# Optimization experiments

Hardware: AMD Instinct MI355X
Metric: run time of the kernel (lower is better)

Reference implementation:

```python
import jax, jax.numpy as jnp
import numpy as np

B, H, C, W = 16, 256, 128, 128  # input is (B, H, C_in, W); C_out = C_in = 128


def setup_inputs() -> dict:
    key = jax.random.key(0)
    ks = jax.random.split(key, 7)
    s = 0.02
    return {
        "x": jax.random.normal(ks[0], (B, H, C, W), dtype=jnp.float32),
        "Wq": jax.random.normal(ks[1], (C, C), dtype=jnp.float32) * s,
        "bq": jnp.zeros((C,), dtype=jnp.float32),
        "Wk": jax.random.normal(ks[2], (C, C), dtype=jnp.float32) * s,
        "bk": jnp.zeros((C,), dtype=jnp.float32),
        "Wv": jax.random.normal(ks[3], (C, C), dtype=jnp.float32) * s,
        "bv": jnp.zeros((C,), dtype=jnp.float32),
        "Wn": jax.random.normal(ks[4], (C, C), dtype=jnp.float32) * s,
        "bn": jnp.zeros((C,), dtype=jnp.float32),
        "Wo": jax.random.normal(ks[5], (C, C), dtype=jnp.float32) * s,
        "bo": jnp.zeros((C,), dtype=jnp.float32),
    }


def reference(x, Wq, bq, Wk, bk, Wv, bv, Wn, bn, Wo, bo):
    # x: (B, H, C, W) -> channels_first layout (B, C, H, W)
    xt = jnp.transpose(x, (0, 2, 1, 3))
    # 1x1 channels_first convs == channel-mixing GEMMs
    q = jnp.einsum('bchw,cd->bdhw', xt, Wq) + bq[None, :, None, None]
    k = jnp.einsum('bchw,cd->bdhw', xt, Wk) + bk[None, :, None, None]
    v = jnp.einsum('bchw,cd->bdhw', xt, Wv) + bv[None, :, None, None]
    # QK^T over H, laid out as (B, C, C', W); scale by sqrt(W) (= last dim of k)
    scale = jnp.sqrt(jnp.asarray(k.shape[-1], dtype=x.dtype))
    scores = jnp.einsum('bchw,bdhw->bcdw', q, k) / scale
    attn = jax.nn.softmax(scores, axis=-1)  # softmax over W axis (as in source)
    # DropConnect: identity at inference (training=None)
    # weight_norm: channels_last 1x1 conv mixing the second C axis
    wn = jnp.einsum('bcdw,de->bcew', attn, Wn) + bn[None, None, :, None]
    # attention-value matmul: out[b,c,h,w] = sum_d wn[b,c,d,w] * v[b,d,h,w]
    m = jnp.einsum('bcdw,bdhw->bchw', wn, v)
    # conv1: channels_first 1x1, C_in -> C_out
    out = jnp.einsum('bchw,co->bohw', m, Wo) + bo[None, :, None, None]
    # back to (B, H, C_out, W)
    return jnp.transpose(out, (0, 2, 1, 3))
```

## Files before the change

kernel.cpp:

```cpp
#include <hip/hip_runtime.h>
#include <cstddef>

#define BB 16
#define HH 256
#define CC 128
#define WW 128

typedef _Float16 f16;
typedef _Float16 f16x8 __attribute__((ext_vector_type(8)));
typedef _Float16 f16x4 __attribute__((ext_vector_type(4)));
typedef _Float16 f16x2 __attribute__((ext_vector_type(2)));
typedef float f32x4 __attribute__((ext_vector_type(4)));

#define LD1 136
#define LDX 264
#define REG 17920

__device__ __forceinline__ void zero_acc(f32x4 acc[4][4]) {
#pragma unroll
    for (int i = 0; i < 4; ++i)
#pragma unroll
        for (int j = 0; j < 4; ++j) acc[i][j] = (f32x4){0.f, 0.f, 0.f, 0.f};
}

__device__ __forceinline__ void gemm_ab(const f16* __restrict__ A, int lda,
                                        const f16* __restrict__ B, int ldb,
                                        int K, int m0, int n0, int l15, int quad,
                                        f32x4 acc[4][4]) {
    for (int kc = 0; kc < K; kc += 32) {
        f16x8 af[4], bf[4];
        const f16* ap = A + (size_t)(m0 + l15) * lda + kc + quad * 8;
        const f16* bp = B + (size_t)(n0 + l15) * ldb + kc + quad * 8;
#pragma unroll
        for (int t = 0; t < 4; ++t) {
            af[t] = *(const f16x8*)(ap + t * 16 * lda);
            bf[t] = *(const f16x8*)(bp + t * 16 * ldb);
        }
#pragma unroll
        for (int mt = 0; mt < 4; ++mt)
#pragma unroll
            for (int nt = 0; nt < 4; ++nt)
                acc[mt][nt] = __builtin_amdgcn_mfma_f32_16x16x32_f16(af[mt], bf[nt], acc[mt][nt], 0, 0, 0);
    }
}

__device__ __forceinline__ void gemm_a_btr(const f16* __restrict__ A, int lda,
                                           const f16* __restrict__ XS,
                                           int m0, int n0, int l15, int quad,
                                           f32x4 acc[4][4]) {
    const unsigned xb = (unsigned)(size_t)XS;
    for (int kc = 0; kc < 128; kc += 32) {
        f16x8 af[4];
        const f16* ap = A + (size_t)(m0 + l15) * lda + kc + quad * 8;
#pragma unroll
        for (int t = 0; t < 4; ++t) af[t] = *(const f16x8*)(ap + t * 16 * lda);
        int i0 = (kc >> 2) + 2 * quad;
        f16x4 blo[4], bhi[4];
#pragma unroll
        for (int nt = 0; nt < 4; ++nt) {
            unsigned idx0 = (unsigned)(i0 * 8 + (n0 >> 4) + nt);
            unsigned a0 = xb + (idx0 * 68u + (unsigned)l15 * 4u) * 2u;
            unsigned a1 = a0 + 8u * 68u * 2u;
            asm volatile("ds_read_b64_tr_b16 %0, %1" : "=v"(blo[nt]) : "v"(a0));
            asm volatile("ds_read_b64_tr_b16 %0, %1" : "=v"(bhi[nt]) : "v"(a1));
        }
        asm volatile("s_waitcnt lgkmcnt(0)" ::: "memory");
        __builtin_amdgcn_sched_barrier(0);
#pragma unroll
        for (int nt = 0; nt < 4; ++nt) {
            f16x8 bv = __builtin_shufflevector(blo[nt], bhi[nt], 0, 1, 2, 3, 4, 5, 6, 7);
#pragma unroll
            for (int mt = 0; mt < 4; ++mt)
                acc[mt][nt] = __builtin_amdgcn_mfma_f32_16x16x32_f16(af[mt], bv, acc[mt][nt], 0, 0, 0);
        }
    }
}

__device__ __forceinline__ void stage_ct(const f32x4 acc[4][4], f16* dst, int ld,
                                         int m0, int n0, int l15, int quad) {
#pragma unroll
    for (int mt = 0; mt < 4; ++mt)
#pragma unroll
        for (int nt = 0; nt < 4; ++nt) {
            f16x4 v;
#pragma unroll
            for (int r = 0; r < 4; ++r) v[r] = (f16)acc[mt][nt][r];
            int col = n0 + nt * 16 + l15;
            int row = m0 + mt * 16 + quad * 4;
            *(f16x4*)(dst + (size_t)col * ld + row) = v;
        }
}

__device__ __forceinline__ void stage_c_mirror(const f32x4 acc[4][4], f16* dst, int ld,
                                               int m0, int n0, int l15, int quad) {
#pragma unroll
    for (int mt = 0; mt < 4; ++mt)
#pragma unroll
        for (int r = 0; r < 4; ++r) {
            int row = m0 + mt * 16 + quad * 4 + r;
#pragma unroll
            for (int nt = 0; nt < 4; ++nt)
                dst[(size_t)row * ld + n0 + nt * 16 + l15] = (f16)acc[mt][nt][r];
        }
}

__device__ __forceinline__ void stage_ct_r1(const f32x4 acc[4][4], f16* dst, int ld,
                                            int m0, int n0, int l15, int quad,
                                            const float* __restrict__ gv,
                                            const float* __restrict__ wv) {
#pragma unroll
    for (int mt = 0; mt < 4; ++mt)
#pragma unroll
        for (int nt = 0; nt < 4; ++nt) {
            int col = n0 + nt * 16 + l15;
            int row0 = m0 + mt * 16 + quad * 4;
            float ws = wv[col];
            f16x4 v;
#pragma unroll
            for (int r = 0; r < 4; ++r) v[r] = (f16)(acc[mt][nt][r] + ws * gv[row0 + r]);
            *(f16x4*)(dst + (size_t)col * ld + row0) = v;
        }
}

__device__ __forceinline__ void stage_w(const f16* __restrict__ g, f16* dst, int tid) {
#pragma unroll
    for (int i = 0; i < 8; ++i) {
        int idx = tid + i * 256;
        int row = idx >> 4, cc = (idx & 15) * 8;
        *(f16x8*)(dst + row * LD1 + cc) = *(const f16x8*)(g + row * 128 + cc);
    }
}

__device__ __forceinline__ void load_w_reg(const f16* __restrict__ g, f16x8 wr[8], int tid) {
#pragma unroll
    for (int i = 0; i < 8; ++i) {
        int idx = tid + i * 256;
        wr[i] = *(const f16x8*)(g + (idx >> 4) * 128 + (idx & 15) * 8);
    }
}
__device__ __forceinline__ void stage_w_from_reg(const f16x8 wr[8], f16* dst, int tid) {
#pragma unroll
    for (int i = 0; i < 8; ++i) {
        int idx = tid + i * 256;
        *(f16x8*)(dst + (idx >> 4) * LD1 + (idx & 15) * 8) = wr[i];
    }
}
__device__ __forceinline__ void load_x_reg(const f16* __restrict__ g, f16x8 wr[8], int tid) {
#pragma unroll
    for (int i = 0; i < 8; ++i) {
        int idx = tid + i * 256;
        wr[i] = *(const f16x8*)(g + (idx >> 4) * 256 + (idx & 15) * 8);
    }
}
__device__ __forceinline__ void stage_x_from_reg(const f16x8 wr[8], f16* dst, int tid) {
#pragma unroll
    for (int i = 0; i < 8; ++i) {
        int idx = tid + i * 256;
        int c2 = idx >> 4, cc = (idx & 15) * 8;
        int off = ((c2 >> 2) * 8 + (cc >> 4)) * 68 + (c2 & 3) * 16 + (cc & 15);
        f16x4 lo, hi;
#pragma unroll
        for (int j = 0; j < 4; ++j) { lo[j] = wr[i][j]; hi[j] = wr[i][4 + j]; }
        *(f16x4*)(dst + off) = lo;
        *(f16x4*)(dst + off + 4) = hi;
    }
}

__global__ __launch_bounds__(256) void prep_w(const float* __restrict__ Wq, const float* __restrict__ Wk,
                                              const float* __restrict__ Wo, f16* __restrict__ out) {
    int id = blockIdx.x * 256 + threadIdx.x;
    int m = id >> 14;
    int r = (id >> 7) & 127, c = id & 127;
    if (m == 0)      out[id] = (f16)Wq[c * 128 + r];
    else if (m == 1) out[id] = (f16)Wk[c * 128 + r];
    else             out[4 * 16384 + (id & 16383)] = (f16)Wo[c * 128 + r];
}

__global__ __launch_bounds__(512) void prep_mv(const float* __restrict__ Wn, const float* __restrict__ Wv,
                                               const float* __restrict__ Wo, const float* __restrict__ bn,
                                               const float* __restrict__ bv,
                                               f16* __restrict__ Wpk, float* __restrict__ Vg) {
    __shared__ f16 As[128 * LD1];
    __shared__ f16 Bs[128 * LD1];
    const int tid = threadIdx.x;
    if (tid < 128) {
        float s = 0.f;
        for (int e = 0; e < 128; ++e) s = fmaf(Wn[tid * 128 + e], bv[e], s);
        Vg[tid] = s;
    } else if (tid < 256) {
        int c = tid - 128;
        float s = 0.f;
        for (int e = 0; e < 128; ++e) s = fmaf(bn[e], Wv[c * 128 + e], s);
        Vg[128 + c] = s;
    } else if (tid < 384) {
        int o = tid - 256;
        float s = 0.f;
        for (int c = 0; c < 128; ++c) s += Wo[c * 128 + o];
        Vg[256 + o] = s;
    } else if (tid == 384) {
        float s = 0.f;
        for (int e = 0; e < 128; ++e) s = fmaf(bn[e], bv[e], s);
        Vg[384] = s;
    }
    if (tid < 256) {
#pragma unroll
        for (int i = 0; i < 8; ++i) {
            int idx = tid + i * 256;
            int r = idx >> 4, c = (idx & 15) * 8;
            f16x8 va, vb;
            const float* pa = Wv + r * 128 + c;
            const float* pb = Wn + r * 128 + c;
#pragma unroll
            for (int j = 0; j < 8; ++j) { va[j] = (f16)pa[j]; vb[j] = (f16)pb[j]; }
            *(f16x8*)(As + r * LD1 + c) = va;
            *(f16x8*)(Bs + r * LD1 + c) = vb;
        }
    }
    __syncthreads();
    if (tid < 256) {
        const int lane = tid & 63, wid = tid >> 6;
        const int l15 = lane & 15, quad = lane >> 4;
        const int m0 = (wid >> 1) * 64, n0 = (wid & 1) * 64;
        f32x4 acc[4][4];
        zero_acc(acc);
        gemm_ab(As, LD1, Bs, LD1, 128, m0, n0, l15, quad, acc);
        f16* Mt = Wpk + 2 * 16384;
#pragma unroll
        for (int mt = 0; mt < 4; ++mt)
#pragma unroll
            for (int r = 0; r < 4; ++r) {
                int cp = m0 + mt * 16 + quad * 4 + r;
#pragma unroll
                for (int nt = 0; nt < 4; ++nt) {
                    int d = n0 + nt * 16 + l15;
                    Mt[cp * 128 + d] = (f16)acc[mt][nt][r];
                }
            }
    }
}

__global__ __launch_bounds__(256) void t1_k(const float* __restrict__ src, f16* __restrict__ dst) {
    __shared__ float tile[64][68];
    int bx = blockIdx.x;
    const int pw = bx & 1;  bx >>= 1;
    const int ph = bx & 3;  bx >>= 2;
    const int c  = bx & 127;
    const int b  = bx >> 7;
    const int tid = threadIdx.x;
    const int h0 = ph * 64, w0 = pw * 64;
    {
        const int r = tid >> 4, c4 = (tid & 15) * 4;
        size_t base = (((size_t)b * HH + h0 + r) * CC + c) * WW + w0 + c4;
#pragma unroll
        for (int k = 0; k < 4; ++k) {
            float4 v = *(const float4*)(src + base + (size_t)(16 * k) * CC * WW);
            *(float4*)&tile[r + 16 * k][c4] = v;
        }
    }
    __syncthreads();
    {
        const int rw = tid >> 3, h8 = (tid & 7) * 8;
        size_t dbase = (((size_t)b * WW + w0 + rw) * CC + c) * HH + h0 + h8;
#pragma unroll
        for (int k = 0; k < 2; ++k) {
            f16x8 v;
#pragma unroll
            for (int j = 0; j < 8; ++j) v[j] = (f16)tile[h8 + j][rw + 32 * k];
            *(f16x8*)(dst + dbase + (size_t)(32 * k) * CC * HH) = v;
        }
    }
}

__global__ __launch_bounds__(256) void t2_k(const f16* __restrict__ src, float* __restrict__ dst) {
    __shared__ float tile[64][68];
    int bx = blockIdx.x;
    const int ct = bx & 1;  bx >>= 1;
    const int wt = bx & 1;  bx >>= 1;
    const int h  = bx & 255;
    const int b  = bx >> 8;
    const int tid = threadIdx.x;
    const int c0 = ct * 64, w0 = wt * 64;
    {
        const int r = tid >> 3, c8 = (tid & 7) * 8;
#pragma unroll
        for (int k = 0; k < 2; ++k) {
            int wr = r + 32 * k;
            f16x8 v = *(const f16x8*)(src + (((size_t)b * WW + w0 + wr) * HH + h) * CC + c0 + c8);
#pragma unroll
            for (int j = 0; j < 8; ++j) tile[wr][c8 + j] = (float)v[j];
        }
    }
    __syncthreads();
    {
        const int rc = tid >> 4, w4 = (tid & 15) * 4;
#pragma unroll
        for (int k = 0; k < 4; ++k) {
            int cr = rc + 16 * k;
            float4 o;
            o.x = tile[w4 + 0][cr]; o.y = tile[w4 + 1][cr];
            o.z = tile[w4 + 2][cr]; o.w = tile[w4 + 3][cr];
            *(float4*)(dst + (((size_t)b * HH + h) * CC + c0 + cr) * WW + w0 + w4) = o;
        }
    }
}

__global__ __launch_bounds__(256, 2) void p1_kernel(const f16* __restrict__ Xt,
                                                    const f16* __restrict__ Wpk,
                                                    const float* __restrict__ Wq_g, const float* __restrict__ bq,
                                                    const float* __restrict__ Wk_g, const float* __restrict__ bk,
                                                    f16* __restrict__ Sout) {
    __shared__ f16 sm[2 * REG];
    __shared__ float rbuf[128], rqb[128], rkb[128];
    const int tid = threadIdx.x;
    const int w = blockIdx.x, b = blockIdx.y;
    const f16* Xg = Xt + (size_t)(b * WW + w) * (CC * HH);
    f16* Xs = sm;
    f16* RA = sm;
    f16* RB = sm + REG;

    f16x8 wkreg[8];
    load_w_reg(Wpk + 1 * 16384, wkreg, tid);

#pragma unroll
    for (int i = 0; i < 16; ++i) {
        int g = tid + i * 256;
        int row = g >> 5, cc = (g & 31) * 8;
        *(f16x8*)(Xs + row * LDX + cc) = *(const f16x8*)(Xg + row * 256 + cc);
    }
    __syncthreads();

    const int lane = tid & 63, wid = tid >> 6;
    const int l15 = lane & 15, quad = lane >> 4;
    const int m0 = (wid >> 1) * 64, n0 = (wid & 1) * 64;

    f32x4 acc[4][4];
    if (wid != 2) {
        zero_acc(acc);
        gemm_ab(Xs, LDX, Xs, LDX, 256, m0, n0, l15, quad, acc);
    } else {
#pragma unroll
        for (int hf = 0; hf < 2; ++hf) {
            int c = lane + 64 * hf;
            float s = 0.f;
            for (int hc = 0; hc < 32; ++hc) {
                f16x8 v = *(const f16x8*)(Xs + (size_t)c * LDX + hc * 8);
#pragma unroll
                for (int j = 0; j < 8; ++j) s += (float)v[j];
            }
            rbuf[c] = s;
        }
    }
    __syncthreads();

    if (wid != 2) stage_ct(acc, RA, LD1, m0, n0, l15, quad);
    if (wid == 1) stage_c_mirror(acc, RA, LD1, m0, n0, l15, quad);
    stage_w(Wpk + 0 * 16384, RB, tid);
    if (tid < 128) {
        float s = 0.f;
        for (int c = 0; c < 128; ++c) s = fmaf(Wq_g[c * 128 + tid], rbuf[c], s);
        rqb[tid] = s;
    } else {
        int d = tid - 128;
        float s = 0.f;
        for (int c = 0; c < 128; ++c) s = fmaf(Wk_g[c * 128 + d], rbuf[c], s);
        rkb[d] = s;
    }
    __syncthreads();

    zero_acc(acc);
    gemm_ab(RA, LD1, RB, LD1, 128, m0, n0, l15, quad, acc);
    __syncthreads();
    stage_ct(acc, RA, LD1, m0, n0, l15, quad);
    stage_w_from_reg(wkreg, RB, tid);
    __syncthreads();

    zero_acc(acc);
    gemm_ab(RA, LD1, RB, LD1, 128, m0, n0, l15, quad, acc);

    const float inv_scale = 0.08838834764831845f;
    f16* Sg = Sout + (size_t)(b * WW + w) * (CC * CC);
#pragma unroll
    for (int mt = 0; mt < 4; ++mt)
#pragma unroll
        for (int r = 0; r < 4; ++r) {
            int dq = m0 + mt * 16 + quad * 4 + r;
            float q1 = bq[dq], q2 = rqb[dq];
#pragma unroll
            for (int nt = 0; nt < 4; ++nt) {
                int dk = n0 + nt * 16 + l15;
                float kb = bk[dk], kr = rkb[dk];
                Sg[dq * 128 + dk] = (f16)((acc[mt][nt][r] + q2 * kb + q1 * kr + 256.f * q1 * kb) * inv_scale);
            }
        }
}

__global__ __launch_bounds__(256) void p2_kernel(const f16* __restrict__ S,
                                                 float* __restrict__ z) {
    int i = (blockIdx.x * 256 + threadIdx.x) * 2;
    int b = i >> 14, cd = i & 16383;
    const f16* p = S + (size_t)b * WW * CC * CC + cd;
    float m0v = -1e30f, l0 = 0.f, m1v = -1e30f, l1 = 0.f;
    for (int w = 0; w < WW; w += 4) {
        f16x2 v0 = *(const f16x2*)(p + (size_t)(w + 0) * CC * CC);
        f16x2 v1 = *(const f16x2*)(p + (size_t)(w + 1) * CC * CC);
        f16x2 v2 = *(const f16x2*)(p + (size_t)(w + 2) * CC * CC);
        f16x2 v3 = *(const f16x2*)(p + (size_t)(w + 3) * CC * CC);
#pragma unroll
        for (int j = 0; j < 4; ++j) {
            f16x2 v = (j == 0) ? v0 : (j == 1) ? v1 : (j == 2) ? v2 : v3;
            float s0 = (float)v[0], s1 = (float)v[1];
            float n0 = fmaxf(m0v, s0), n1 = fmaxf(m1v, s1);
            l0 = fmaf(l0, __expf(m0v - n0), __expf(s0 - n0)); m0v = n0;
            l1 = fmaf(l1, __expf(m1v - n1), __expf(s1 - n1)); m1v = n1;
        }
    }
    z[i]     = m0v + __logf(l0);
    z[i + 1] = m1v + __logf(l1);
}

__global__ __launch_bounds__(256, 2) void p3_kernel(f16* __restrict__ XtO,
                                                    const f16* __restrict__ Sin, const float* __restrict__ Zin,
                                                    const f16* __restrict__ Wpk,
                                                    const float* __restrict__ Vg,
                                                    const float* __restrict__ bo_g) {
    __shared__ f16 sm[2 * REG];
    __shared__ float t1b[128], ub[128], gb[128], wb[128];
    const int tid = threadIdx.x;
    const int w = blockIdx.x, b = blockIdx.y;
    const f16* Sg = Sin + (size_t)(b * WW + w) * (CC * CC);
    const float* Zb = Zin + (size_t)b * (CC * CC);
    f16* Xg = XtO + (size_t)(b * WW + w) * (CC * HH);
    f16* R0 = sm;
    f16* R1 = sm + REG;

    f16x8 wreg[8];
    load_w_reg(Wpk + 4 * 16384, wreg, tid);

    if (tid < 128) { gb[tid] = Vg[128 + tid]; wb[tid] = Vg[256 + tid]; }

#pragma unroll
    for (int i = 0; i < 8; ++i) {
        int g = tid + i * 256;
        int c = g >> 4, d8 = (g & 15) * 8;
        f16x8 s8 = *(const f16x8*)(Sg + c * 128 + d8);
        float4 za = *(const float4*)(Zb + c * 128 + d8);
        float4 zc = *(const float4*)(Zb + c * 128 + d8 + 4);
        f16x8 e;
        e[0] = (f16)__expf((float)s8[0] - za.x);
        e[1] = (f16)__expf((float)s8[1] - za.y);
        e[2] = (f16)__expf((float)s8[2] - za.z);
        e[3] = (f16)__expf((float)s8[3] - za.w);
        e[4] = (f16)__expf((float)s8[4] - zc.x);
        e[5] = (f16)__expf((float)s8[5] - zc.y);
        e[6] = (f16)__expf((float)s8[6] - zc.z);
        e[7] = (f16)__expf((float)s8[7] - zc.w);
        *(f16x8*)(R0 + c * LD1 + d8) = e;
    }
    stage_w(Wpk + 2 * 16384, R1, tid);
    __syncthreads();

    const int lane = tid & 63, wid = tid >> 6;
    const int l15 = lane & 15, quad = lane >> 4;
    const int m0 = (wid >> 1) * 64, n0 = (wid & 1) * 64;

    if (tid < 128) {
        float s = Vg[384];
        for (int d = 0; d < 128; ++d) s = fmaf((float)R0[tid * LD1 + d], Vg[d], s);
        t1b[tid] = s;
    }

    f32x4 acc[4][4];
    zero_acc(acc);
    gemm_ab(R0, LD1, R1, LD1, 128, m0, n0, l15, quad, acc);
    __syncthreads();
    stage_ct(acc, R0, LD1, m0, n0, l15, quad);
    stage_w_from_reg(wreg, R1, tid);
    load_x_reg(Xg, wreg, tid);
    __syncthreads();
    if (tid < 128) {
        float s = 0.f;
        for (int c = 0; c < 128; ++c) s = fmaf((float)R1[tid * LD1 + c], t1b[c], s);
        ub[tid] = s + bo_g[tid];
    }
    zero_acc(acc);
    gemm_ab(R0, LD1, R1, LD1, 128, m0, n0, l15, quad, acc);
    __syncthreads();
    stage_ct_r1(acc, R1, LD1, m0, n0, l15, quad, gb, wb);
    stage_x_from_reg(wreg, R0, tid);
    load_x_reg(Xg + 128, wreg, tid);
    __syncthreads();
    zero_acc(acc);
    gemm_a_btr(R1, LD1, R0, m0, n0, l15, quad, acc);
#pragma unroll
    for (int mt = 0; mt < 4; ++mt)
#pragma unroll
        for (int nt = 0; nt < 4; ++nt) {
            int h = n0 + nt * 16 + l15;
            int o = m0 + mt * 16 + quad * 4;
            f16x4 v;
#pragma unroll
            for (int r = 0; r < 4; ++r) v[r] = (f16)(acc[mt][nt][r] + ub[o + r]);
            *(f16x4*)(Xg + h * 128 + o) = v;
        }
    __syncthreads();
    stage_x_from_reg(wreg, R0, tid);
    __syncthreads();
    zero_acc(acc);
    gemm_a_btr(R1, LD1, R0, m0, n0, l15, quad, acc);
#pragma unroll
    for (int mt = 0; mt < 4; ++mt)
#pragma unroll
        for (int nt = 0; nt < 4; ++nt) {
            int h = 128 + n0 + nt * 16 + l15;
            int o = m0 + mt * 16 + quad * 4;
            f16x4 v;
#pragma unroll
            for (int r = 0; r < 4; ++r) v[r] = (f16)(acc[mt][nt][r] + ub[o + r]);
            *(f16x4*)(Xg + h * 128 + o) = v;
        }
}

extern "C" void kernel_launch(void* const* d_in, const int* in_sizes, int n_in,
                              void* d_out, int out_size, void* d_ws, size_t ws_size,
                              hipStream_t stream) {
    const float* x  = (const float*)d_in[0];
    const float* Wq = (const float*)d_in[1];
    const float* bq = (const float*)d_in[2];
    const float* Wk = (const float*)d_in[3];
    const float* bk = (const float*)d_in[4];
    const float* Wv = (const float*)d_in[5];
    const float* bv = (const float*)d_in[6];
    const float* Wn = (const float*)d_in[7];
    const float* bn = (const float*)d_in[8];
    const float* Wo = (const float*)d_in[9];
    const float* bo = (const float*)d_in[10];
    float* out = (float*)d_out;

    f16*   wsX = (f16*)d_ws;
    f16*   wsS = (f16*)((char*)d_ws + 134217728);
    float* wsV = (float*)((char*)d_ws + 134217728 + 67108864);
    float* wsZ = (float*)((char*)d_ws + 268435456);
    f16*   wsW = (f16*)((char*)d_ws + 268435456 + 1048576);

    prep_w<<<192, 256, 0, stream>>>(Wq, Wk, Wo, wsW);
    prep_mv<<<1, 512, 0, stream>>>(Wn, Wv, Wo, bn, bv, wsW, wsV);
    t1_k<<<BB * CC * 4 * 2, 256, 0, stream>>>(x, wsX);
    p1_kernel<<<dim3(WW, BB), 256, 0, stream>>>(wsX, wsW, Wq, bq, Wk, bk, wsS);
    p2_kernel<<<(BB * CC * CC) / 512, 256, 0, stream>>>(wsS, wsZ);
    p3_kernel<<<dim3(WW, BB), 256, 0, stream>>>(wsX, wsS, wsZ, wsW, wsV, bo);
    t2_k<<<BB * 256 * 2 * 2, 256, 0, stream>>>(wsX, out);
}
```

Measured before the change: 691.2 us.

## Double block size to 512 threads in p1/p3 with 64x32 per-wave MFMA tiles

Raises p1_kernel and p3_kernel (and prep_mv's GEMM) from 256 to 512 threads, so each of 8 waves computes a 64x32 output tile instead of 64x64. Row-sum and bias matvecs that previously ran on a subset of threads are now spread across all threads with shuffle reductions. In p1 the gram matrix is computed in full instead of using a symmetric mirror copy, and the Wk register prefetch is moved later. The aim is more waves to hide LDS and global latency and to cut serial scalar work. In exchange, each wave reuses fewer B fragments per A load, and the tighter launch bounds may limit registers.

```diff
diff --git a/kernel.cpp b/kernel.cpp
--- a/kernel.cpp
+++ b/kernel.cpp
@@ -16,30 +16,29 @@
 #define LDX 264
 #define REG 17920
 
-__device__ __forceinline__ void zero_acc(f32x4 acc[4][4]) {
+__device__ __forceinline__ void zero_acc(f32x4 acc[4][2]) {
 #pragma unroll
     for (int i = 0; i < 4; ++i)
 #pragma unroll
-        for (int j = 0; j < 4; ++j) acc[i][j] = (f32x4){0.f, 0.f, 0.f, 0.f};
+        for (int j = 0; j < 2; ++j) acc[i][j] = (f32x4){0.f, 0.f, 0.f, 0.f};
 }
 
 __device__ __forceinline__ void gemm_ab(const f16* __restrict__ A, int lda,
                                         const f16* __restrict__ B, int ldb,
                                         int K, int m0, int n0, int l15, int quad,
-                                        f32x4 acc[4][4]) {
+                                        f32x4 acc[4][2]) {
     for (int kc = 0; kc < K; kc += 32) {
-        f16x8 af[4], bf[4];
+        f16x8 af[4], bf[2];
         const f16* ap = A + (size_t)(m0 + l15) * lda + kc + quad * 8;
         const f16* bp = B + (size_t)(n0 + l15) * ldb + kc + quad * 8;
 #pragma unroll
-        for (int t = 0; t < 4; ++t) {
-            af[t] = *(const f16x8*)(ap + t * 16 * lda);
-            bf[t] = *(const f16x8*)(bp + t * 16 * ldb);
-        }
+        for (int t = 0; t < 4; ++t) af[t] = *(const f16x8*)(ap + t * 16 * lda);
+#pragma unroll
+        for (int t = 0; t < 2; ++t) bf[t] = *(const f16x8*)(bp + t * 16 * ldb);
 #pragma unroll
         for (int mt = 0; mt < 4; ++mt)
 #pragma unroll
-            for (int nt = 0; nt < 4; ++nt)
+            for (int nt = 0; nt < 2; ++nt)
                 acc[mt][nt] = __builtin_amdgcn_mfma_f32_16x16x32_f16(af[mt], bf[nt], acc[mt][nt], 0, 0, 0);
     }
 }
@@ -47,7 +46,7 @@
 __device__ __forceinline__ void gemm_a_btr(const f16* __restrict__ A, int lda,
                                            const f16* __restrict__ XS,
                                            int m0, int n0, int l15, int quad,
-                                           f32x4 acc[4][4]) {
+                                           f32x4 acc[4][2]) {
     const unsigned xb = (unsigned)(size_t)XS;
     for (int kc = 0; kc < 128; kc += 32) {
         f16x8 af[4];
@@ -55,9 +54,9 @@
 #pragma unroll
         for (int t = 0; t < 4; ++t) af[t] = *(const f16x8*)(ap + t * 16 * lda);
         int i0 = (kc >> 2) + 2 * quad;
-        f16x4 blo[4], bhi[4];
-#pragma unroll
-        for (int nt = 0; nt < 4; ++nt) {
+        f16x4 blo[2], bhi[2];
+#pragma unroll
+        for (int nt = 0; nt < 2; ++nt) {
             unsigned idx0 = (unsigned)(i0 * 8 + (n0 >> 4) + nt);
             unsigned a0 = xb + (idx0 * 68u + (unsigned)l15 * 4u) * 2u;
             unsigned a1 = a0 + 8u * 68u * 2u;
@@ -67,7 +66,7 @@
         asm volatile("s_waitcnt lgkmcnt(0)" ::: "memory");
         __builtin_amdgcn_sched_barrier(0);
 #pragma unroll
-        for (int nt = 0; nt < 4; ++nt) {
+        for (int nt = 0; nt < 2; ++nt) {
             f16x8 bv = __builtin_shufflevector(blo[nt], bhi[nt], 0, 1, 2, 3, 4, 5, 6, 7);
 #pragma unroll
             for (int mt = 0; mt < 4; ++mt)
@@ -76,12 +75,12 @@
     }
 }
 
-__device__ __forceinline__ void stage_ct(const f32x4 acc[4][4], f16* dst, int ld,
+__device__ __forceinline__ void stage_ct(const f32x4 acc[4][2], f16* dst, int ld,
                                          int m0, int n0, int l15, int quad) {
 #pragma unroll
     for (int mt = 0; mt < 4; ++mt)
 #pragma unroll
-        for (int nt = 0; nt < 4; ++nt) {
+        for (int nt = 0; nt < 2; ++nt) {
             f16x4 v;
 #pragma unroll
             for (int r = 0; r < 4; ++r) v[r] = (f16)acc[mt][nt][r];
@@ -91,27 +90,14 @@
         }
 }
 
-__device__ __forceinline__ void stage_c_mirror(const f32x4 acc[4][4], f16* dst, int ld,
-                                               int m0, int n0, int l15, int quad) {
-#pragma unroll
-    for (int mt = 0; mt < 4; ++mt)
-#pragma unroll
-        for (int r = 0; r < 4; ++r) {
-            int row = m0 + mt * 16 + quad * 4 + r;
-#pragma unroll
-            for (int nt = 0; nt < 4; ++nt)
-                dst[(size_t)row * ld + n0 + nt * 16 + l15] = (f16)acc[mt][nt][r];
-        }
-}
-
-__device__ __forceinline__ void stage_ct_r1(const f32x4 acc[4][4], f16* dst, int ld,
+__device__ __forceinline__ void stage_ct_r1(const f32x4 acc[4][2], f16* dst, int ld,
                                             int m0, int n0, int l15, int quad,
                                             const float* __restrict__ gv,
                                             const float* __restrict__ wv) {
 #pragma unroll
     for (int mt = 0; mt < 4; ++mt)
 #pragma unroll
-        for (int nt = 0; nt < 4; ++nt) {
+        for (int nt = 0; nt < 2; ++nt) {
             int col = n0 + nt * 16 + l15;
             int row0 = m0 + mt * 16 + quad * 4;
             float ws = wv[col];
@@ -124,38 +110,38 @@
 
 __device__ __forceinline__ void stage_w(const f16* __restrict__ g, f16* dst, int tid) {
 #pragma unroll
-    for (int i = 0; i < 8; ++i) {
-        int idx = tid + i * 256;
+    for (int i = 0; i < 4; ++i) {
+        int idx = tid + i * 512;
         int row = idx >> 4, cc = (idx & 15) * 8;
         *(f16x8*)(dst + row * LD1 + cc) = *(const f16x8*)(g + row * 128 + cc);
     }
 }
 
-__device__ __forceinline__ void load_w_reg(const f16* __restrict__ g, f16x8 wr[8], int tid) {
-#pragma unroll
-    for (int i = 0; i < 8; ++i) {
-        int idx = tid + i * 256;
+__device__ __forceinline__ void load_w_reg(const f16* __restrict__ g, f16x8 wr[4], int tid) {
+#pragma unroll
+    for (int i = 0; i < 4; ++i) {
+        int idx = tid + i * 512;
         wr[i] = *(const f16x8*)(g + (idx >> 4) * 128 + (idx & 15) * 8);
     }
 }
-__device__ __forceinline__ void stage_w_from_reg(const f16x8 wr[8], f16* dst, int tid) {
-#pragma unroll
-    for (int i = 0; i < 8; ++i) {
-        int idx = tid + i * 256;
+__device__ __forceinline__ void stage_w_from_reg(const f16x8 wr[4], f16* dst, int tid) {
+#pragma unroll
+    for (int i = 0; i < 4; ++i) {
+        int idx = tid + i * 512;
         *(f16x8*)(dst + (idx >> 4) * LD1 + (idx & 15) * 8) = wr[i];
     }
 }
-__device__ __forceinline__ void load_x_reg(const f16* __restrict__ g, f16x8 wr[8], int tid) {
-#pragma unroll
-    for (int i = 0; i < 8; ++i) {
-        int idx = tid + i * 256;
+__device__ __forceinline__ void load_x_reg(const f16* __restrict__ g, f16x8 wr[4], int tid) {
+#pragma unroll
+    for (int i = 0; i < 4; ++i) {
+        int idx = tid + i * 512;
         wr[i] = *(const f16x8*)(g + (idx >> 4) * 256 + (idx & 15) * 8);
     }
 }
-__device__ __forceinline__ void stage_x_from_reg(const f16x8 wr[8], f16* dst, int tid) {
-#pragma unroll
-    for (int i = 0; i < 8; ++i) {
-        int idx = tid + i * 256;
+__device__ __forceinline__ void stage_x_from_reg(const f16x8 wr[4], f16* dst, int tid) {
+#pragma unroll
+    for (int i = 0; i < 4; ++i) {
+        int idx = tid + i * 512;
         int c2 = idx >> 4, cc = (idx & 15) * 8;
         int off = ((c2 >> 2) * 8 + (cc >> 4)) * 68 + (c2 & 3) * 16 + (cc & 15);
         f16x4 lo, hi;
@@ -202,41 +188,37 @@
         for (int e = 0; e < 128; ++e) s = fmaf(bn[e], bv[e], s);
         Vg[384] = s;
     }
-    if (tid < 256) {
-#pragma unroll
-        for (int i = 0; i < 8; ++i) {
-            int idx = tid + i * 256;
-            int r = idx >> 4, c = (idx & 15) * 8;
-            f16x8 va, vb;
-            const float* pa = Wv + r * 128 + c;
-            const float* pb = Wn + r * 128 + c;
-#pragma unroll
-            for (int j = 0; j < 8; ++j) { va[j] = (f16)pa[j]; vb[j] = (f16)pb[j]; }
-            *(f16x8*)(As + r * LD1 + c) = va;
-            *(f16x8*)(Bs + r * LD1 + c) = vb;
-        }
-    }
-    __syncthreads();
-    if (tid < 256) {
-        const int lane = tid & 63, wid = tid >> 6;
-        const int l15 = lane & 15, quad = lane >> 4;
-        const int m0 = (wid >> 1) * 64, n0 = (wid & 1) * 64;
-        f32x4 acc[4][4];
-        zero_acc(acc);
-        gemm_ab(As, LD1, Bs, LD1, 128, m0, n0, l15, quad, acc);
-        f16* Mt = Wpk + 2 * 16384;
-#pragma unroll
-        for (int mt = 0; mt < 4; ++mt)
-#pragma unroll
-            for (int r = 0; r < 4; ++r) {
-                int cp = m0 + mt * 16 + quad * 4 + r;
-#pragma unroll
-                for (int nt = 0; nt < 4; ++nt) {
-                    int d = n0 + nt * 16 + l15;
-                    Mt[cp * 128 + d] = (f16)acc[mt][nt][r];
-                }
+#pragma unroll
+    for (int i = 0; i < 4; ++i) {
+        int idx = tid + i * 512;
+        int r = idx >> 4, c = (idx & 15) * 8;
+        f16x8 va, vb;
+        const float* pa = Wv + r * 128 + c;
+        const float* pb = Wn + r * 128 + c;
+#pragma unroll
+        for (int j = 0; j < 8; ++j) { va[j] = (f16)pa[j]; vb[j] = (f16)pb[j]; }
+        *(f16x8*)(As + r * LD1 + c) = va;
+        *(f16x8*)(Bs + r * LD1 + c) = vb;
+    }
+    __syncthreads();
+    const int lane = tid & 63, wid = tid >> 6;
+    const int l15 = lane & 15, quad = lane >> 4;
+    const int m0 = (wid >> 2) * 64, n0 = (wid & 3) * 32;
+    f32x4 acc[4][2];
+    zero_acc(acc);
+    gemm_ab(As, LD1, Bs, LD1, 128, m0, n0, l15, quad, acc);
+    f16* Mt = Wpk + 2 * 16384;
+#pragma unroll
+    for (int mt = 0; mt < 4; ++mt)
+#pragma unroll
+        for (int r = 0; r < 4; ++r) {
+            int cp = m0 + mt * 16 + quad * 4 + r;
+#pragma unroll
+            for (int nt = 0; nt < 2; ++nt) {
+                int d = n0 + nt * 16 + l15;
+                Mt[cp * 128 + d] = (f16)acc[mt][nt][r];
             }
-    }
+        }
 }
 
 __global__ __launch_bounds__(256) void t1_k(const float* __restrict__ src, f16* __restrict__ dst) {
@@ -304,7 +286,7 @@
     }
 }
 
-__global__ __launch_bounds__(256, 2) void p1_kernel(const f16* __restrict__ Xt,
+__global__ __launch_bounds__(512, 4) void p1_kernel(const f16* __restrict__ Xt,
                                                     const f16* __restrict__ Wpk,
                                                     const float* __restrict__ Wq_g, const float* __restrict__ bq,
                                                     const float* __restrict__ Wk_g, const float* __restrict__ bk,
@@ -318,12 +300,9 @@
     f16* RA = sm;
     f16* RB = sm + REG;
 
-    f16x8 wkreg[8];
-    load_w_reg(Wpk + 1 * 16384, wkreg, tid);
-
-#pragma unroll
-    for (int i = 0; i < 16; ++i) {
-        int g = tid + i * 256;
+#pragma unroll
+    for (int i = 0; i < 8; ++i) {
+        int g = tid + i * 512;
         int row = g >> 5, cc = (g & 31) * 8;
         *(f16x8*)(Xs + row * LDX + cc) = *(const f16x8*)(Xg + row * 256 + cc);
     }
@@ -331,45 +310,52 @@
 
     const int lane = tid & 63, wid = tid >> 6;
     const int l15 = lane & 15, quad = lane >> 4;
-    const int m0 = (wid >> 1) * 64, n0 = (wid & 1) * 64;
-
-    f32x4 acc[4][4];
-    if (wid != 2) {
-        zero_acc(acc);
-        gemm_ab(Xs, LDX, Xs, LDX, 256, m0, n0, l15, quad, acc);
-    } else {
-#pragma unroll
-        for (int hf = 0; hf < 2; ++hf) {
-            int c = lane + 64 * hf;
+    const int m0 = (wid >> 2) * 64, n0 = (wid & 3) * 32;
+
+    {
+        int c = tid >> 2, q = tid & 3;
+        float s = 0.f;
+        const f16* xr = Xs + (size_t)c * LDX + q * 64;
+#pragma unroll
+        for (int k = 0; k < 8; ++k) {
+            f16x8 v = *(const f16x8*)(xr + k * 8);
+#pragma unroll
+            for (int j = 0; j < 8; ++j) s += (float)v[j];
+        }
+        s += __shfl_xor(s, 1); s += __shfl_xor(s, 2);
+        if (q == 0) rbuf[c] = s;
+    }
+    f32x4 acc[4][2];
+    zero_acc(acc);
+    gemm_ab(Xs, LDX, Xs, LDX, 256, m0, n0, l15, quad, acc);
+    __syncthreads();
+
+    stage_ct(acc, RA, LD1, m0, n0, l15, quad);
+    stage_w(Wpk + 0 * 16384, RB, tid);
+    __syncthreads();
+
+    f16x8 wkreg[4];
+    load_w_reg(Wpk + 1 * 16384, wkreg, tid);
+    {
+        int hf = tid & 1;
+        if (tid < 256) {
+            int d = tid >> 1;
             float s = 0.f;
-            for (int hc = 0; hc < 32; ++hc) {
-                f16x8 v = *(const f16x8*)(Xs + (size_t)c * LDX + hc * 8);
-#pragma unroll
-                for (int j = 0; j < 8; ++j) s += (float)v[j];
-            }
-            rbuf[c] = s;
-        }
-    }
-    __syncthreads();
-
-    if (wid != 2) stage_ct(acc, RA, LD1, m0, n0, l15, quad);
-    if (wid == 1) stage_c_mirror(acc, RA, LD1, m0, n0, l15, quad);
-    stage_w(Wpk + 0 * 16384, RB, tid);
-    if (tid < 128) {
-        float s = 0.f;
-        for (int c = 0; c < 128; ++c) s = fmaf(Wq_g[c * 128 + tid], rbuf[c], s);
-        rqb[tid] = s;
-    } else {
-        int d = tid - 128;
-        float s = 0.f;
-        for (int c = 0; c < 128; ++c) s = fmaf(Wk_g[c * 128 + d], rbuf[c], s);
-        rkb[d] = s;
-    }
-    __syncthreads();
-
+            for (int c = hf * 64; c < hf * 64 + 64; ++c) s = fmaf(Wq_g[c * 128 + d], rbuf[c], s);
+            s += __shfl_xor(s, 1);
+            if (!hf) rqb[d] = s;
+        } else {
+            int d = (tid - 256) >> 1;
+            float s = 0.f;
+            for (int c = hf * 64; c < hf * 64 + 64; ++c) s = fmaf(Wk_g[c * 128 + d], rbuf[c], s);
+            s += __shfl_xor(s, 1);
+            if (!hf) rkb[d] = s;
+        }
+    }
     zero_acc(acc);
     gemm_ab(RA, LD1, RB, LD1, 128, m0, n0, l15, quad, acc);
     __syncthreads();
+
     stage_ct(acc, RA, LD1, m0, n0, l15, quad);
     stage_w_from_reg(wkreg, RB, tid);
     __syncthreads();
@@ -386,7 +372,7 @@
             int dq = m0 + mt * 16 + quad * 4 + r;
             float q1 = bq[dq], q2 = rqb[dq];
 #pragma unroll
-            for (int nt = 0; nt < 4; ++nt) {
+            for (int nt = 0; nt < 2; ++nt) {
                 int dk = n0 + nt * 16 + l15;
                 float kb = bk[dk], kr = rkb[dk];
                 Sg[dq * 128 + dk] = (f16)((acc[mt][nt][r] + q2 * kb + q1 * kr + 256.f * q1 * kb) * inv_scale);
@@ -418,13 +404,13 @@
     z[i + 1] = m1v + __logf(l1);
 }
 
-__global__ __launch_bounds__(256, 2) void p3_kernel(f16* __restrict__ XtO,
+__global__ __launch_bounds__(512, 4) void p3_kernel(f16* __restrict__ XtO,
                                                     const f16* __restrict__ Sin, const float* __restrict__ Zin,
                                                     const f16* __restrict__ Wpk,
                                                     const float* __restrict__ Vg,
                                                     const float* __restrict__ bo_g) {
     __shared__ f16 sm[2 * REG];
-    __shared__ float t1b[128], ub[128], gb[128], wb[128];
+    __shared__ float t1b[128], ub[128], gb[128], wb[128], h1b[128];
     const int tid = threadIdx.x;
     const int w = blockIdx.x, b = blockIdx.y;
     const f16* Sg = Sin + (size_t)(b * WW + w) * (CC * CC);
@@ -433,14 +419,10 @@
     f16* R0 = sm;
     f16* R1 = sm + REG;
 
-    f16x8 wreg[8];
-    load_w_reg(Wpk + 4 * 16384, wreg, tid);
-
-    if (tid < 128) { gb[tid] = Vg[128 + tid]; wb[tid] = Vg[256 + tid]; }
-
-#pragma unroll
-    for (int i = 0; i < 8; ++i) {
-        int g = tid + i * 256;
+    if (tid < 128) { gb[tid] = Vg[128 + tid]; wb[tid] = Vg[256 + tid]; h1b[tid] = Vg[tid]; }
+#pragma unroll
+    for (int i = 0; i < 4; ++i) {
+        int g = tid + i * 512;
         int c = g >> 4, d8 = (g & 15) * 8;
         f16x8 s8 = *(const f16x8*)(Sg + c * 128 + d8);
         float4 za = *(const float4*)(Zb + c * 128 + d8);
@@ -461,40 +443,62 @@
 
     const int lane = tid & 63, wid = tid >> 6;
     const int l15 = lane & 15, quad = lane >> 4;
-    const int m0 = (wid >> 1) * 64, n0 = (wid & 1) * 64;
-
-    if (tid < 128) {
-        float s = Vg[384];
-        for (int d = 0; d < 128; ++d) s = fmaf((float)R0[tid * LD1 + d], Vg[d], s);
-        t1b[tid] = s;
-    }
-
-    f32x4 acc[4][4];
+    const int m0 = (wid >> 2) * 64, n0 = (wid & 3) * 32;
+
+    f16x8 wreg[4];
+    load_w_reg(Wpk + 4 * 16384, wreg, tid);
+    float s0v = Vg[384];
+    {
+        int c = tid >> 2, q = tid & 3;
+        float s = 0.f;
+        const f16* ar = R0 + (size_t)c * LD1 + q * 32;
+#pragma unroll
+        for (int k = 0; k < 4; ++k) {
+            f16x8 v = *(const f16x8*)(ar + k * 8);
+#pragma unroll
+            for (int j = 0; j < 8; ++j) s = fmaf((float)v[j], h1b[q * 32 + k * 8 + j], s);
+        }
+        s += __shfl_xor(s, 1); s += __shfl_xor(s, 2);
+        if (q == 0) t1b[c] = s + s0v;
+    }
+    f32x4 acc[4][2];
     zero_acc(acc);
     gemm_ab(R0, LD1, R1, LD1, 128, m0, n0, l15, quad, acc);
     __syncthreads();
+
     stage_ct(acc, R0, LD1, m0, n0, l15, quad);
     stage_w_from_reg(wreg, R1, tid);
     load_x_reg(Xg, wreg, tid);
     __syncthreads();
-    if (tid < 128) {
-        float s = 0.f;
-        for (int c = 0; c < 128; ++c) s = fmaf((float)R1[tid * LD1 + c], t1b[c], s);
-        ub[tid] = s + bo_g[tid];
+
+    {
+        int o = tid >> 2, q = tid & 3;
+        float s = 0.f;
+        const f16* wr_ = R1 + (size_t)o * LD1 + q * 32;
+#pragma unroll
+        for (int k = 0; k < 4; ++k) {
+            f16x8 v = *(const f16x8*)(wr_ + k * 8);
+#pragma unroll
+            for (int j = 0; j < 8; ++j) s = fmaf((float)v[j], t1b[q * 32 + k * 8 + j], s);
+        }
+        s += __shfl_xor(s, 1); s += __shfl_xor(s, 2);
+        if (q == 0) ub[o] = s + bo_g[o];
     }
     zero_acc(acc);
     gemm_ab(R0, LD1, R1, LD1, 128, m0, n0, l15, quad, acc);
     __syncthreads();
+
     stage_ct_r1(acc, R1, LD1, m0, n0, l15, quad, gb, wb);
     stage_x_from_reg(wreg, R0, tid);
     load_x_reg(Xg + 128, wreg, tid);
     __syncthreads();
+
     zero_acc(acc);
     gemm_a_btr(R1, LD1, R0, m0, n0, l15, quad, acc);
 #pragma unroll
     for (int mt = 0; mt < 4; ++mt)
 #pragma unroll
-        for (int nt = 0; nt < 4; ++nt) {
+        for (int nt = 0; nt < 2; ++nt) {
             int h = n0 + nt * 16 + l15;
             int o = m0 + mt * 16 + quad * 4;
             f16x4 v;
@@ -503,14 +507,16 @@
             *(f16x4*)(Xg + h * 128 + o) = v;
         }
     __syncthreads();
+
     stage_x_from_reg(wreg, R0, tid);
     __syncthreads();
+
     zero_acc(acc);
     gemm_a_btr(R1, LD1, R0, m0, n0, l15, quad, acc);
 #pragma unroll
     for (int mt = 0; mt < 4; ++mt)
 #pragma unroll
-        for (int nt = 0; nt < 4; ++nt) {
+        for (int nt = 0; nt < 2; ++nt) {
             int h = 128 + n0 + nt * 16 + l15;
             int o = m0 + mt * 16 + quad * 4;
             f16x4 v;
@@ -545,8 +551,8 @@
     prep_w<<<192, 256, 0, stream>>>(Wq, Wk, Wo, wsW);
     prep_mv<<<1, 512, 0, stream>>>(Wn, Wv, Wo, bn, bv, wsW, wsV);
     t1_k<<<BB * CC * 4 * 2, 256, 0, stream>>>(x, wsX);
-    p1_kernel<<<dim3(WW, BB), 256, 0, stream>>>(wsX, wsW, Wq, bq, Wk, bk, wsS);
+    p1_kernel<<<dim3(WW, BB), 512, 0, stream>>>(wsX, wsW, Wq, bq, Wk, bk, wsS);
     p2_kernel<<<(BB * CC * CC) / 512, 256, 0, stream>>>(wsS, wsZ);
-    p3_kernel<<<dim3(WW, BB), 256, 0, stream>>>(wsX, wsS, wsZ, wsW, wsV, bo);
+    p3_kernel<<<dim3(WW, BB), 512, 0, stream>>>(wsX, wsS, wsZ, wsW, wsV, bo);
     t2_k<<<BB * 256 * 2 * 2, 256, 0, stream>>>(wsX, out);
 }
```

Result: slower. 708.8 us (+2.5%).
